# Kernel tuning notes

Measured on AMD Instinct MI355X. Metric: run time of the kernel, lower is better.

## Reference

```python
import jax, jax.numpy as jnp
import numpy as np

B, S, D, H = 2, 2048, 1024, 16
HD = D // H
WIN = 32
LN_EPS = 1e-5


def _ln(x, g, b):
    m = jnp.mean(x, axis=-1, keepdims=True)
    v = jnp.mean(jnp.square(x - m), axis=-1, keepdims=True)
    return (x - m) / jnp.sqrt(v + LN_EPS) * g + b


def setup_inputs() -> dict:
    key = jax.random.key(0)
    ks = jax.random.split(key, 12)
    def w(k, shape):
        return jax.random.normal(k, shape, dtype=jnp.float32) * 0.02
    inp = {
        'x': jax.random.normal(ks[0], (B, S, D), dtype=jnp.float32),
        'fq_w': w(ks[1], (D, D)), 'fq_b': jnp.zeros((D,), jnp.float32),
        'fk_w': w(ks[2], (D, D)), 'fk_b': jnp.zeros((D,), jnp.float32),
        'fv_w': w(ks[3], (D, D)), 'fv_b': jnp.zeros((D,), jnp.float32),
        'bq_w': w(ks[4], (D, D)), 'bq_b': jnp.zeros((D,), jnp.float32),
        'bk_w': w(ks[5], (D, D)), 'bk_b': jnp.zeros((D,), jnp.float32),
        'bv_w': w(ks[6], (D, D)), 'bv_b': jnp.zeros((D,), jnp.float32),
        'gate_w': w(ks[7], (2 * D, D)), 'gate_b': jnp.zeros((D,), jnp.float32),
        'gln_g': jnp.ones((D,), jnp.float32), 'gln_b': jnp.zeros((D,), jnp.float32),
        'bstr': jnp.asarray(0.1, jnp.float32),
        'out_w': w(ks[8], (D, D)), 'out_b': jnp.zeros((D,), jnp.float32),
        'ln_g': jnp.ones((D,), jnp.float32), 'ln_b': jnp.zeros((D,), jnp.float32),
    }
    return inp


def _heads(x, w, b):
    # [B,S,D] -> [B,H,S,HD]
    y = x @ w + b
    return y.reshape(B, S, H, HD).transpose(0, 2, 1, 3)


def _merge(x):
    return x.transpose(0, 2, 1, 3).reshape(B, S, D)


def _forward(x, fq_w, fq_b, fk_w, fk_b, fv_w, fv_b,
             bq_w, bq_b, bk_w, bk_b, bv_w, bv_b,
             gate_w, gate_b, gln_g, gln_b, bstr, out_w, out_b, ln_g, ln_b):
    scale = 1.0 / np.sqrt(HD)
    i = jnp.arange(S)
    # --- causal forward attention ---
    Q = _heads(x, fq_w, fq_b); K = _heads(x, fk_w, fk_b); V = _heads(x, fv_w, fv_b)
    scores = jnp.einsum('bhqd,bhkd->bhqk', Q, K) * scale
    causal = i[:, None] >= i[None, :]  # allowed positions
    scores = jnp.where(causal[None, None], scores, -jnp.inf)
    fwd = _merge(jnp.einsum('bhqk,bhkd->bhqd', jax.nn.softmax(scores, axis=-1), V))
    # --- limited-window backward attention (future_context = hidden_states) ---
    Qb = _heads(x, bq_w, bq_b); Kb = _heads(x, bk_w, bk_b); Vb = _heads(x, bv_w, bv_b)
    sb = jnp.einsum('bhqd,bhkd->bhqk', Qb, Kb) * scale
    valid = (i[None, :] > i[:, None]) & (i[None, :] <= i[:, None] + WIN)
    sb = jnp.where(valid[None, None], sb, -jnp.inf)
    # rows with no valid future (last row) get scores reset to 0 -> uniform softmax,
    # matching torch's all_masked handling
    row_valid = valid.any(axis=-1)  # [S]
    sb = jnp.where(row_valid[None, None, :, None], sb, 0.0)
    bwd = _merge(jnp.einsum('bhqk,bhkd->bhqd', jax.nn.softmax(sb, axis=-1), Vb))
    # --- weak gated fusion (eval mode: no dropout, backward detached) ---
    combined = jnp.concatenate([fwd, bwd], axis=-1)
    gate = jax.nn.sigmoid(_ln(combined @ gate_w + gate_b, gln_g, gln_b))
    strength = jax.nn.sigmoid(bstr) * 0.3
    fused = fwd + strength * gate * jax.lax.stop_gradient(bwd)
    out = fused @ out_w + out_b
    return _ln(x + out, ln_g, ln_b)


def reference(x, fq_w, fq_b, fk_w, fk_b, fv_w, fv_b,
              bq_w, bq_b, bk_w, bk_b, bv_w, bv_b,
              gate_w, gate_b, gln_g, gln_b, bstr, out_w, out_b, ln_g, ln_b):
    return _forward(x, fq_w, fq_b, fk_w, fk_b, fv_w, fv_b,
                    bq_w, bq_b, bk_w, bk_b, bv_w, bv_b,
                    gate_w, gate_b, gln_g, gln_b, bstr, out_w, out_b, ln_g, ln_b)
```

## Files before the change

kernel.cpp:

```cpp
#include <hip/hip_runtime.h>

#define S_LEN 2048
#define NH 16
#define HD 64
#define DMODEL 1024
#define NTOK 4096
#define ELTS_PER 4194304
#define QSCALE 0.18033688f

typedef __attribute__((ext_vector_type(8))) __bf16 bfrag;
typedef __attribute__((ext_vector_type(8))) short s8v;
typedef __attribute__((ext_vector_type(4))) float f32x4;

__device__ inline float bf2f(short s) {
  unsigned int u = ((unsigned int)(unsigned short)s) << 16;
  float f;
  __builtin_memcpy(&f, &u, 4);
  return f;
}
__device__ inline short f2bf(float f) {
  unsigned int u;
  __builtin_memcpy(&u, &f, 4);
  u = (u + 0x7fffu + ((u >> 16) & 1u)) >> 16;
  return (short)u;
}
__device__ inline short f2bf_n(float f) {
  __bf16 h = (__bf16)f;
  short s;
  __builtin_memcpy(&s, &h, 2);
  return s;
}
__device__ inline float bflo(unsigned int u) {
  unsigned int t = u << 16;
  float f; __builtin_memcpy(&f, &t, 4); return f;
}
__device__ inline float bfhi(unsigned int u) {
  unsigned int t = u & 0xffff0000u;
  float f; __builtin_memcpy(&f, &t, 4); return f;
}
__device__ __forceinline__ void gll16(const short* g, short* l) {
  __builtin_amdgcn_global_load_lds(
      (const __attribute__((address_space(1))) void*)g,
      (__attribute__((address_space(3))) void*)l, 16, 0, 0);
}

__global__ __launch_bounds__(256) void cvt_bf16_kernel(const float* __restrict__ in,
                                                       short* __restrict__ out, int n) {
  int i = (blockIdx.x * 256 + threadIdx.x) * 4;
  if (i + 3 < n) {
    float4 v = *reinterpret_cast<const float4*>(in + i);
    short4 o;
    o.x = f2bf(v.x); o.y = f2bf(v.y); o.z = f2bf(v.z); o.w = f2bf(v.w);
    *reinterpret_cast<short4*>(out + i) = o;
  }
}

__global__ void transpose_cvt_all(const float* __restrict__ s0, const float* __restrict__ s1,
                                  const float* __restrict__ s2, const float* __restrict__ s3,
                                  const float* __restrict__ s4, const float* __restrict__ s5,
                                  const float* __restrict__ s6, const float* __restrict__ s7,
                                  short* d0, short* d1, short* d2, short* d3,
                                  short* d4, short* d5, short* d6, short* d7) {
  const int z = blockIdx.z;
  const int K = (z == 7) ? 2048 : 1024;
  if (blockIdx.y * 32 >= K) return;
  const float* srcs[8] = {s0, s1, s2, s3, s4, s5, s6, s7};
  short* dsts[8] = {d0, d1, d2, d3, d4, d5, d6, d7};
  const float* in = srcs[z];
  short* out = dsts[z];
  __shared__ float tile[32][33];
  int nb = blockIdx.x * 32, kb = blockIdx.y * 32;
  int tx = threadIdx.x, ty = threadIdx.y;
  for (int j = 0; j < 32; j += 8)
    tile[ty + j][tx] = in[(size_t)(kb + ty + j) * 1024 + nb + tx];
  __syncthreads();
  for (int j = 0; j < 32; j += 8)
    out[(size_t)(nb + ty + j) * K + kb + tx] = f2bf(tile[tx][ty + j]);
}

__global__ __launch_bounds__(256) void gemm_qkv_kernel(
    const short* __restrict__ A, int lda, int K,
    const short* __restrict__ B0, const short* __restrict__ B1, const short* __restrict__ B2,
    const short* __restrict__ B3, const short* __restrict__ B4, const short* __restrict__ B5,
    const float* __restrict__ bias0, const float* __restrict__ bias1,
    const float* __restrict__ bias2, const float* __restrict__ bias3,
    const float* __restrict__ bias4, const float* __restrict__ bias5,
    short* __restrict__ outQ) {
  __shared__ short lds[128 * 136];
  short* As = lds;
  short* Bs = lds + 8192;
  const int tid = threadIdx.x;
  const int n0 = blockIdx.x * 128;
  const int m0 = blockIdx.y * 128;
  const short* Bp[6] = {B0, B1, B2, B3, B4, B5};
  const float* biasP[6] = {bias0, bias1, bias2, bias3, bias4, bias5};
  const int nsel = n0 >> 10;
  const int nc0 = n0 & 1023;
  const short* Bt = Bp[nsel] + (size_t)nc0 * K;
  const float* bsel = biasP[nsel];

  const int lane = tid & 63;
  const int w = tid >> 6;
  const int wm = (w >> 1) * 64;
  const int wn = (w & 1) * 64;
  const int lr = lane & 15;
  const int lg = lane >> 4;
  const int rl = lane >> 3;
  const int gch = (lane & 7) ^ (rl & 7);

  f32x4 acc[4][4];
  for (int a = 0; a < 4; ++a)
    for (int b = 0; b < 4; ++b) acc[a][b] = {0.f, 0.f, 0.f, 0.f};

  for (int k0 = 0; k0 < K; k0 += 64) {
    __syncthreads();
    for (int p = 0; p < 4; ++p) {
      int rb = (p * 4 + w) * 8;
      gll16(A + (size_t)(m0 + rb + rl) * lda + k0 + gch * 8, &As[rb * 64]);
      gll16(Bt + (size_t)(rb + rl) * K + k0 + gch * 8, &Bs[rb * 64]);
    }
    __syncthreads();
    for (int ks = 0; ks < 2; ++ks) {
      bfrag af[4], bf[4];
      for (int t = 0; t < 4; ++t) {
        af[t] = *reinterpret_cast<const bfrag*>(
            &As[(wm + t * 16 + lr) * 64 + (((lg + 4 * ks) ^ (lr & 7)) * 8)]);
        bf[t] = *reinterpret_cast<const bfrag*>(
            &Bs[(wn + t * 16 + lr) * 64 + (((lg + 4 * ks) ^ (lr & 7)) * 8)]);
      }
      for (int mt = 0; mt < 4; ++mt)
        for (int nt = 0; nt < 4; ++nt)
          acc[mt][nt] = __builtin_amdgcn_mfma_f32_16x16x32_bf16(af[mt], bf[nt], acc[mt][nt], 0, 0, 0);
    }
  }

  const float cmul = (nsel == 0 || nsel == 3) ? QSCALE : 1.0f;
  const bool tr = (nsel == 2 || nsel == 5);
  __syncthreads();
  for (int mt = 0; mt < 4; ++mt)
    for (int nt = 0; nt < 4; ++nt) {
      int c = wn + nt * 16 + lr;
      float bv = bsel[nc0 + c];
      for (int i = 0; i < 4; ++i) {
        int r = wm + mt * 16 + lg * 4 + i;
        short v16 = f2bf_n((acc[mt][nt][i] + bv) * cmul);
        if (tr) lds[c * 136 + r] = v16;
        else lds[r * 136 + c] = v16;
      }
    }
  __syncthreads();
  const int bb = m0 >> 11;
  const int sloc = m0 & 2047;
  const int hh0 = nc0 >> 6;
  short* basebuf = outQ + (size_t)nsel * ELTS_PER;
  for (int j = 0; j < 8; ++j) {
    int gid = j * 256 + tid;
    int rr = gid >> 4;
    int ch = gid & 15;
    s8v v = *reinterpret_cast<const s8v*>(&lds[rr * 136 + ch * 8]);
    if (tr) {
      int hh = hh0 + (rr >> 6), d = rr & 63;
      *reinterpret_cast<s8v*>(
          basebuf + ((size_t)(bb * NH + hh) * HD + d) * S_LEN + sloc + ch * 8) = v;
    } else {
      int hh = hh0 + (ch >> 3), d0 = (ch & 7) * 8;
      *reinterpret_cast<s8v*>(
          basebuf + ((size_t)(bb * NH + hh) * S_LEN + sloc + rr) * HD + d0) = v;
    }
  }
}

__global__ __launch_bounds__(256) void gemm_ksplit_kernel(
    const short* __restrict__ A0, const short* __restrict__ A1, int lda,
    const short* __restrict__ B, int ldb, int K,
    const float* __restrict__ bias, float* __restrict__ out0, float* __restrict__ out1) {
  __shared__ short lds[16384];
  short* As = lds;
  short* Bs = lds + 8192;
  const int tid = threadIdx.x;
  const int n0 = blockIdx.x * 128;
  const int m0 = blockIdx.y * 128;
  const int z = blockIdx.z;
  const short* A = z ? A1 : A0;
  const short* Bt = B + (size_t)n0 * ldb + z * K;
  float* outp = z ? out1 : out0;

  const int lane = tid & 63;
  const int w = tid >> 6;
  const int wm = (w >> 1) * 64;
  const int wn = (w & 1) * 64;
  const int lr = lane & 15;
  const int lg = lane >> 4;
  const int rl = lane >> 3;
  const int gch = (lane & 7) ^ (rl & 7);

  f32x4 acc[4][4];
  for (int a = 0; a < 4; ++a)
    for (int b = 0; b < 4; ++b) acc[a][b] = {0.f, 0.f, 0.f, 0.f};

  for (int k0 = 0; k0 < K; k0 += 64) {
    __syncthreads();
    for (int p = 0; p < 4; ++p) {
      int rb = (p * 4 + w) * 8;
      gll16(A + (size_t)(m0 + rb + rl) * lda + k0 + gch * 8, &As[rb * 64]);
      gll16(Bt + (size_t)(rb + rl) * ldb + k0 + gch * 8, &Bs[rb * 64]);
    }
    __syncthreads();
    for (int ks = 0; ks < 2; ++ks) {
      bfrag af[4], bf[4];
      for (int t = 0; t < 4; ++t) {
        af[t] = *reinterpret_cast<const bfrag*>(
            &As[(wm + t * 16 + lr) * 64 + (((lg + 4 * ks) ^ (lr & 7)) * 8)]);
        bf[t] = *reinterpret_cast<const bfrag*>(
            &Bs[(wn + t * 16 + lr) * 64 + (((lg + 4 * ks) ^ (lr & 7)) * 8)]);
      }
      for (int mt = 0; mt < 4; ++mt)
        for (int nt = 0; nt < 4; ++nt)
          acc[mt][nt] = __builtin_amdgcn_mfma_f32_16x16x32_bf16(af[mt], bf[nt], acc[mt][nt], 0, 0, 0);
    }
  }

  for (int mt = 0; mt < 4; ++mt)
    for (int nt = 0; nt < 4; ++nt)
      for (int i = 0; i < 4; ++i) {
        int row = m0 + wm + mt * 16 + lg * 4 + i;
        int col = n0 + wn + nt * 16 + lr;
        float v = acc[mt][nt][i] + (z == 0 ? bias[col] : 0.f);
        outp[(size_t)row * DMODEL + col] = v;
      }
}

__global__ __launch_bounds__(256) void attn_fwd_kernel(const short* __restrict__ Q,
                                                       const short* __restrict__ Kk,
                                                       const short* __restrict__ VT,
                                                       short* __restrict__ fwd) {
  __shared__ short Kls[64 * 64];
  __shared__ short Vls[64 * 64];
  __shared__ short Ps[4][32 * 72];
  const int tid = threadIdx.x;
  const int lane = tid & 63;
  const int w = tid >> 6;
  const int lr = lane & 15;
  const int lg = lane >> 4;
  const int f = blockIdx.x;
  const int xcd = f & 7;
  const int s = f >> 3;
  const int bhl = s & 3;
  const int t = s >> 2;
  const int j = (t < 8) ? t : (23 - t);
  const int bh = xcd * 4 + bhl;
  const int b = bh >> 4;
  const int h = bh & 15;
  const size_t hb = (size_t)bh * S_LEN * HD;
  short* Pw = Ps[w];

  s8v onesi = {0x3F80, 0x3F80, 0x3F80, 0x3F80, 0x3F80, 0x3F80, 0x3F80, 0x3F80};
  bfrag onesv;
  __builtin_memcpy(&onesv, &onesi, 16);

  const int q0 = j * 128 + w * 32;
  const int ktmax = 2 * j + 1;

  const int rl8 = lane >> 3;
  const int gch = (lane & 7) ^ rl8;

  bfrag qf[2][2];
  for (int mt = 0; mt < 2; ++mt)
    for (int kc = 0; kc < 2; ++kc)
      qf[mt][kc] = *reinterpret_cast<const bfrag*>(
          Q + hb + (size_t)(q0 + mt * 16 + lr) * HD + kc * 32 + lg * 8);

  f32x4 oacc[2][4];
  for (int mt = 0; mt < 2; ++mt)
    for (int nd = 0; nd < 4; ++nd) oacc[mt][nd] = {0.f, 0.f, 0.f, 0.f};
  f32x4 osum[2];
  osum[0] = {0.f, 0.f, 0.f, 0.f};
  osum[1] = {0.f, 0.f, 0.f, 0.f};

  for (int kt = 0; kt <= ktmax; ++kt) {
    __syncthreads();
    const short* Kg = Kk + hb + (size_t)(kt * 64 + w * 16 + rl8) * HD + gch * 8;
    gll16(Kg, &Kls[(w * 16) * 64]);
    gll16(Kg + (size_t)8 * HD, &Kls[(w * 16 + 8) * 64]);
    const short* Vg = VT + hb + (size_t)(w * 16 + rl8) * S_LEN + kt * 64 + gch * 8;
    gll16(Vg, &Vls[(w * 16) * 64]);
    gll16(Vg + (size_t)8 * S_LEN, &Vls[(w * 16 + 8) * 64]);
    __syncthreads();
    bfrag kf[4][2];
    for (int nb = 0; nb < 4; ++nb)
      for (int kc = 0; kc < 2; ++kc)
        kf[nb][kc] = *reinterpret_cast<const bfrag*>(
            &Kls[(nb * 16 + lr) * 64 + (((kc * 4 + lg) ^ (lr & 7)) * 8)]);
    f32x4 sv[2][4];
    for (int mt = 0; mt < 2; ++mt)
      for (int nb = 0; nb < 4; ++nb) {
        f32x4 z = {0.f, 0.f, 0.f, 0.f};
        z = __builtin_amdgcn_mfma_f32_16x16x32_bf16(qf[mt][0], kf[nb][0], z, 0, 0, 0);
        sv[mt][nb] = __builtin_amdgcn_mfma_f32_16x16x32_bf16(qf[mt][1], kf[nb][1], z, 0, 0, 0);
      }
    if (kt * 64 + 63 > q0) {
      for (int mt = 0; mt < 2; ++mt)
        for (int nb = 0; nb < 4; ++nb)
          for (int i = 0; i < 4; ++i) {
            int colg = kt * 64 + nb * 16 + lr;
            int rowg = q0 + mt * 16 + lg * 4 + i;
            if (colg > rowg) sv[mt][nb][i] = -1e30f;
          }
    }
    for (int mt = 0; mt < 2; ++mt)
      for (int nb = 0; nb < 4; ++nb)
        for (int i = 0; i < 4; ++i)
          Pw[(mt * 16 + lg * 4 + i) * 72 + nb * 16 + lr] = f2bf_n(exp2f(sv[mt][nb][i]));
    bfrag vf[4][2];
    for (int nd = 0; nd < 4; ++nd)
      for (int kc = 0; kc < 2; ++kc)
        vf[nd][kc] = *reinterpret_cast<const bfrag*>(
            &Vls[(nd * 16 + lr) * 64 + (((kc * 4 + lg) ^ (lr & 7)) * 8)]);
    for (int mt = 0; mt < 2; ++mt) {
      bfrag pa0 = *reinterpret_cast<const bfrag*>(&Pw[(mt * 16 + lr) * 72 + lg * 8]);
      bfrag pa1 = *reinterpret_cast<const bfrag*>(&Pw[(mt * 16 + lr) * 72 + 32 + lg * 8]);
      for (int nd = 0; nd < 4; ++nd) {
        oacc[mt][nd] = __builtin_amdgcn_mfma_f32_16x16x32_bf16(pa0, vf[nd][0], oacc[mt][nd], 0, 0, 0);
        oacc[mt][nd] = __builtin_amdgcn_mfma_f32_16x16x32_bf16(pa1, vf[nd][1], oacc[mt][nd], 0, 0, 0);
      }
      osum[mt] = __builtin_amdgcn_mfma_f32_16x16x32_bf16(pa0, onesv, osum[mt], 0, 0, 0);
      osum[mt] = __builtin_amdgcn_mfma_f32_16x16x32_bf16(pa1, onesv, osum[mt], 0, 0, 0);
    }
  }

  for (int mt = 0; mt < 2; ++mt)
    for (int i = 0; i < 4; ++i) {
      int rowg = q0 + mt * 16 + lg * 4 + i;
      float inv = 1.0f / osum[mt][i];
      for (int nd = 0; nd < 4; ++nd)
        fwd[(size_t)(b * S_LEN + rowg) * DMODEL + h * HD + nd * 16 + lr] =
            f2bf(oacc[mt][nd][i] * inv);
    }
}

__global__ __launch_bounds__(256) void attn_bwd_kernel(const short* __restrict__ Qb,
                                                       const short* __restrict__ Kb,
                                                       const short* __restrict__ VT,
                                                       short* __restrict__ bwd) {
  __shared__ short Ps[4][32 * 72];
  const int tid = threadIdx.x;
  const int lane = tid & 63;
  const int w = tid >> 6;
  const int lr = lane & 15;
  const int lg = lane >> 4;
  const int h = blockIdx.y;
  const int b = blockIdx.z;
  const size_t hb = (size_t)(b * NH + h) * S_LEN * HD;
  const int q0 = blockIdx.x * 128 + w * 32;
  short* Pw = Ps[w];

  bfrag qf[2][2];
  for (int mt = 0; mt < 2; ++mt)
    for (int kc = 0; kc < 2; ++kc)
      qf[mt][kc] = *reinterpret_cast<const bfrag*>(
          Qb + hb + (size_t)(q0 + mt * 16 + lr) * HD + kc * 32 + lg * 8);
  bfrag kf[4][2];
  for (int nb = 0; nb < 4; ++nb) {
    int kr = q0 + nb * 16 + lr;
    kr = min(kr, S_LEN - 1);
    for (int kc = 0; kc < 2; ++kc)
      kf[nb][kc] = *reinterpret_cast<const bfrag*>(
          Kb + hb + (size_t)kr * HD + kc * 32 + lg * 8);
  }
  f32x4 sv[2][4];
  for (int mt = 0; mt < 2; ++mt)
    for (int nb = 0; nb < 4; ++nb) {
      f32x4 z = {0.f, 0.f, 0.f, 0.f};
      z = __builtin_amdgcn_mfma_f32_16x16x32_bf16(qf[mt][0], kf[nb][0], z, 0, 0, 0);
      sv[mt][nb] = __builtin_amdgcn_mfma_f32_16x16x32_bf16(qf[mt][1], kf[nb][1], z, 0, 0, 0);
    }
  float mx[2][4];
  for (int mt = 0; mt < 2; ++mt)
    for (int i = 0; i < 4; ++i) {
      int rowg = q0 + mt * 16 + lg * 4 + i;
      float m = -1e30f;
      for (int nb = 0; nb < 4; ++nb) {
        int colg = q0 + nb * 16 + lr;
        float t = sv[mt][nb][i];
        bool valid = (colg > rowg) && (colg <= rowg + 32) && (colg < S_LEN);
        if (!valid) t = -1e30f;
        sv[mt][nb][i] = t;
        m = fmaxf(m, t);
      }
      mx[mt][i] = m;
    }
  for (int off = 1; off < 16; off <<= 1)
    for (int mt = 0; mt < 2; ++mt)
      for (int i = 0; i < 4; ++i) mx[mt][i] = fmaxf(mx[mt][i], __shfl_xor(mx[mt][i], off));
  float rs[2][4] = {{0.f, 0.f, 0.f, 0.f}, {0.f, 0.f, 0.f, 0.f}};
  for (int mt = 0; mt < 2; ++mt)
    for (int nb = 0; nb < 4; ++nb)
      for (int i = 0; i < 4; ++i) {
        float p = exp2f(sv[mt][nb][i] - mx[mt][i]);
        rs[mt][i] += p;
        Pw[(mt * 16 + lg * 4 + i) * 72 + nb * 16 + lr] = f2bf_n(p);
      }
  for (int off = 1; off < 16; off <<= 1)
    for (int mt = 0; mt < 2; ++mt)
      for (int i = 0; i < 4; ++i) rs[mt][i] += __shfl_xor(rs[mt][i], off);
  bfrag vf[4][2];
  for (int nd = 0; nd < 4; ++nd)
    for (int kc = 0; kc < 2; ++kc) {
      int sbase = q0 + kc * 32 + lg * 8;
      sbase = min(sbase, S_LEN - 8);
      vf[nd][kc] = *reinterpret_cast<const bfrag*>(
          VT + hb + (size_t)(nd * 16 + lr) * S_LEN + sbase);
    }
  f32x4 oacc[2][4];
  for (int mt = 0; mt < 2; ++mt)
    for (int nd = 0; nd < 4; ++nd) oacc[mt][nd] = {0.f, 0.f, 0.f, 0.f};
  for (int mt = 0; mt < 2; ++mt) {
    bfrag pa0 = *reinterpret_cast<const bfrag*>(&Pw[(mt * 16 + lr) * 72 + lg * 8]);
    bfrag pa1 = *reinterpret_cast<const bfrag*>(&Pw[(mt * 16 + lr) * 72 + 32 + lg * 8]);
    for (int nd = 0; nd < 4; ++nd) {
      oacc[mt][nd] = __builtin_amdgcn_mfma_f32_16x16x32_bf16(pa0, vf[nd][0], oacc[mt][nd], 0, 0, 0);
      oacc[mt][nd] = __builtin_amdgcn_mfma_f32_16x16x32_bf16(pa1, vf[nd][1], oacc[mt][nd], 0, 0, 0);
    }
  }
  for (int mt = 0; mt < 2; ++mt)
    for (int nd = 0; nd < 4; ++nd)
      for (int i = 0; i < 4; ++i) {
        int rowg = q0 + mt * 16 + lg * 4 + i;
        float ov = oacc[mt][nd][i] / rs[mt][i];
        bwd[(size_t)(b * S_LEN + rowg) * DMODEL + h * HD + nd * 16 + lr] = f2bf(ov);
      }
}

__global__ __launch_bounds__(256) void vmean_kernel(const short* __restrict__ VT,
                                                    short* __restrict__ bwd) {
  __shared__ float red[256];
  const int bh = blockIdx.x;
  const int d = threadIdx.x >> 2;
  const int seg = threadIdx.x & 3;
  const short* row = VT + (size_t)bh * S_LEN * HD + (size_t)d * S_LEN + seg * 512;
  float s = 0.f;
  for (int j = 0; j < 512; j += 8) {
    uint4 v = *reinterpret_cast<const uint4*>(row + j);
    s += bflo(v.x) + bfhi(v.x) + bflo(v.y) + bfhi(v.y) +
         bflo(v.z) + bfhi(v.z) + bflo(v.w) + bfhi(v.w);
  }
  red[threadIdx.x] = s;
  __syncthreads();
  if (seg == 0) {
    float t = red[d * 4] + red[d * 4 + 1] + red[d * 4 + 2] + red[d * 4 + 3];
    int b = bh >> 4, h = bh & 15;
    bwd[((size_t)(b * S_LEN + S_LEN - 1)) * DMODEL + h * HD + d] = f2bf(t * (1.f / S_LEN));
  }
}

__global__ __launch_bounds__(256) void ln_gate_fuse_kernel(
    const float* __restrict__ g0p, const float* __restrict__ g1p,
    const float* __restrict__ gln_g, const float* __restrict__ gln_b,
    const short* __restrict__ fwd, const short* __restrict__ bwd,
    const float* __restrict__ bstr, short* __restrict__ fused) {
  __shared__ float red[8];
  const int row = blockIdx.x;
  const int tid = threadIdx.x;
  const int lane = tid & 63;
  const int w = tid >> 6;
  float4 x0 = *reinterpret_cast<const float4*>(g0p + (size_t)row * DMODEL + tid * 4);
  float4 x1 = *reinterpret_cast<const float4*>(g1p + (size_t)row * DMODEL + tid * 4);
  float xa[4] = {x0.x + x1.x, x0.y + x1.y, x0.z + x1.z, x0.w + x1.w};
  float s = xa[0] + xa[1] + xa[2] + xa[3];
  float ss = xa[0] * xa[0] + xa[1] * xa[1] + xa[2] * xa[2] + xa[3] * xa[3];
  for (int off = 1; off < 64; off <<= 1) {
    s += __shfl_xor(s, off);
    ss += __shfl_xor(ss, off);
  }
  if (lane == 0) { red[w] = s; red[4 + w] = ss; }
  __syncthreads();
  s = red[0] + red[1] + red[2] + red[3];
  ss = red[4] + red[5] + red[6] + red[7];
  const float mean = s * (1.f / DMODEL);
  const float var = ss * (1.f / DMODEL) - mean * mean;
  const float rstd = rsqrtf(var + 1e-5f);
  const float strength = 0.3f / (1.f + __expf(-bstr[0]));
  for (int e = 0; e < 4; ++e) {
    int idx = tid * 4 + e;
    float g = (xa[e] - mean) * rstd * gln_g[idx] + gln_b[idx];
    float gate = 1.f / (1.f + __expf(-g));
    float f = bf2f(fwd[(size_t)row * DMODEL + idx]) +
              strength * gate * bf2f(bwd[(size_t)row * DMODEL + idx]);
    fused[(size_t)row * DMODEL + idx] = f2bf(f);
  }
}

__global__ __launch_bounds__(256) void final_ln_kernel(const float* __restrict__ x,
                                                       const float* __restrict__ o0p,
                                                       const float* __restrict__ o1p,
                                                       const float* __restrict__ ln_g,
                                                       const float* __restrict__ ln_b,
                                                       float* __restrict__ y) {
  __shared__ float red[8];
  const int row = blockIdx.x;
  const int tid = threadIdx.x;
  const int lane = tid & 63;
  const int w = tid >> 6;
  float4 xv = *reinterpret_cast<const float4*>(x + (size_t)row * DMODEL + tid * 4);
  float4 o0 = *reinterpret_cast<const float4*>(o0p + (size_t)row * DMODEL + tid * 4);
  float4 o1 = *reinterpret_cast<const float4*>(o1p + (size_t)row * DMODEL + tid * 4);
  float t[4] = {xv.x + o0.x + o1.x, xv.y + o0.y + o1.y,
                xv.z + o0.z + o1.z, xv.w + o0.w + o1.w};
  float s = t[0] + t[1] + t[2] + t[3];
  float ss = t[0] * t[0] + t[1] * t[1] + t[2] * t[2] + t[3] * t[3];
  for (int off = 1; off < 64; off <<= 1) {
    s += __shfl_xor(s, off);
    ss += __shfl_xor(ss, off);
  }
  if (lane == 0) { red[w] = s; red[4 + w] = ss; }
  __syncthreads();
  s = red[0] + red[1] + red[2] + red[3];
  ss = red[4] + red[5] + red[6] + red[7];
  const float mean = s * (1.f / DMODEL);
  const float var = ss * (1.f / DMODEL) - mean * mean;
  const float rstd = rsqrtf(var + 1e-5f);
  for (int e = 0; e < 4; ++e) {
    int idx = tid * 4 + e;
    y[(size_t)row * DMODEL + idx] = (t[e] - mean) * rstd * ln_g[idx] + ln_b[idx];
  }
}

extern "C" void kernel_launch(void* const* d_in, const int* in_sizes, int n_in,
                              void* d_out, int out_size, void* d_ws, size_t ws_size,
                              hipStream_t stream) {
  const float* x = (const float*)d_in[0];
  const float* fq_w = (const float*)d_in[1];
  const float* fq_b = (const float*)d_in[2];
  const float* fk_w = (const float*)d_in[3];
  const float* fk_b = (const float*)d_in[4];
  const float* fv_w = (const float*)d_in[5];
  const float* fv_b = (const float*)d_in[6];
  const float* bq_w = (const float*)d_in[7];
  const float* bq_b = (const float*)d_in[8];
  const float* bk_w = (const float*)d_in[9];
  const float* bk_b = (const float*)d_in[10];
  const float* bv_w = (const float*)d_in[11];
  const float* bv_b = (const float*)d_in[12];
  const float* gate_w = (const float*)d_in[13];
  const float* gate_b = (const float*)d_in[14];
  const float* gln_g = (const float*)d_in[15];
  const float* gln_b = (const float*)d_in[16];
  const float* bstr = (const float*)d_in[17];
  const float* out_w = (const float*)d_in[18];
  const float* out_b = (const float*)d_in[19];
  const float* ln_g = (const float*)d_in[20];
  const float* ln_b = (const float*)d_in[21];

  char* ws = (char*)d_ws;
  const size_t MB = 1u << 20;
  short* xb = (short*)(ws + 0);
  short* wT0 = (short*)(ws + 8 * MB);
  short* wT1 = (short*)(ws + 10 * MB);
  short* wT2 = (short*)(ws + 12 * MB);
  short* wT3 = (short*)(ws + 14 * MB);
  short* wT4 = (short*)(ws + 16 * MB);
  short* wT5 = (short*)(ws + 18 * MB);
  short* gwT = (short*)(ws + 20 * MB);
  short* owT = (short*)(ws + 24 * MB);
  short* qkv = (short*)(ws + 26 * MB);
  short* fwd = (short*)(ws + 0);
  short* bwdb = (short*)(ws + 8 * MB);
  float* G0 = (float*)(ws + 26 * MB);
  float* G1 = (float*)(ws + 42 * MB);
  short* fused = (short*)(ws + 58 * MB);
  float* O0 = (float*)(ws + 26 * MB);
  float* O1 = (float*)(ws + 42 * MB);

  cvt_bf16_kernel<<<4096, 256, 0, stream>>>(x, xb, ELTS_PER);
  transpose_cvt_all<<<dim3(32, 64, 8), dim3(32, 8), 0, stream>>>(
      fq_w, fk_w, fv_w, bq_w, bk_w, bv_w, out_w, gate_w,
      wT0, wT1, wT2, wT3, wT4, wT5, owT, gwT);

  gemm_qkv_kernel<<<dim3(48, 32), 256, 0, stream>>>(
      xb, 1024, 1024, wT0, wT1, wT2, wT3, wT4, wT5,
      fq_b, fk_b, fv_b, bq_b, bk_b, bv_b, qkv);

  attn_fwd_kernel<<<512, 256, 0, stream>>>(
      qkv, qkv + (size_t)ELTS_PER, qkv + 2 * (size_t)ELTS_PER, fwd);
  attn_bwd_kernel<<<dim3(16, 16, 2), 256, 0, stream>>>(
      qkv + 3 * (size_t)ELTS_PER, qkv + 4 * (size_t)ELTS_PER, qkv + 5 * (size_t)ELTS_PER, bwdb);
  vmean_kernel<<<32, 256, 0, stream>>>(qkv + 5 * (size_t)ELTS_PER, bwdb);

  gemm_ksplit_kernel<<<dim3(8, 32, 2), 256, 0, stream>>>(
      fwd, bwdb, 1024, gwT, 2048, 1024, gate_b, G0, G1);

  ln_gate_fuse_kernel<<<4096, 256, 0, stream>>>(G0, G1, gln_g, gln_b, fwd, bwdb, bstr, fused);

  gemm_ksplit_kernel<<<dim3(8, 32, 2), 256, 0, stream>>>(
      fused, fused + 512, 1024, owT, 1024, 512, out_b, O0, O1);

  final_ln_kernel<<<4096, 256, 0, stream>>>(x, O0, O1, ln_g, ln_b, (float*)d_out);
}
```

Baseline: 250.9 us.

## Double-buffer LDS tiles in GEMM and forward attention kernels

The QKV and k-split GEMMs move from a single 64-wide K tile to double-buffered 32-wide K tiles, with a new XOR swizzle. The next tile is prefetched with global-to-LDS loads while MFMAs run on the current one, leaving one barrier per iteration instead of two. The causal forward attention kernel likewise double-buffers its K/V tiles to overlap loads with compute. The cost is twice the LDS for attention K/V and twice as many loop iterations with less MFMA work each in the GEMMs, which could raise barrier overhead.

After: 261.6 us. 1.04x slower.

```diff
diff --git a/kernel.cpp b/kernel.cpp
--- a/kernel.cpp
+++ b/kernel.cpp
@@ -87,8 +87,6 @@
     const float* __restrict__ bias4, const float* __restrict__ bias5,
     short* __restrict__ outQ) {
   __shared__ short lds[128 * 136];
-  short* As = lds;
-  short* Bs = lds + 8192;
   const int tid = threadIdx.x;
   const int n0 = blockIdx.x * 128;
   const int m0 = blockIdx.y * 128;
@@ -105,38 +103,46 @@
   const int wn = (w & 1) * 64;
   const int lr = lane & 15;
   const int lg = lane >> 4;
-  const int rl = lane >> 3;
-  const int gch = (lane & 7) ^ (rl & 7);
+  const int gr = lane >> 2;
+  const int gs = (((lane & 3) ^ ((gr >> 1) & 3)) * 8);
+  const int rsw = (lr >> 1) & 3;
 
   f32x4 acc[4][4];
   for (int a = 0; a < 4; ++a)
     for (int b = 0; b < 4; ++b) acc[a][b] = {0.f, 0.f, 0.f, 0.f};
 
-  for (int k0 = 0; k0 < K; k0 += 64) {
+#define QKV_STAGE(K0, AD, BD)                                              \
+  do {                                                                     \
+    const short* Ag = A + (size_t)(m0 + w * 32 + gr) * lda + (K0) + gs;    \
+    gll16(Ag, (AD) + (w * 32) * 32);                                       \
+    gll16(Ag + (size_t)16 * lda, (AD) + (w * 32 + 16) * 32);               \
+    const short* Bg = Bt + (size_t)(w * 32 + gr) * K + (K0) + gs;          \
+    gll16(Bg, (BD) + (w * 32) * 32);                                       \
+    gll16(Bg + (size_t)16 * K, (BD) + (w * 32 + 16) * 32);                 \
+  } while (0)
+
+  QKV_STAGE(0, lds, lds + 8192);
+  __syncthreads();
+  for (int k0 = 0; k0 < K; k0 += 32) {
+    const int cur = (k0 >> 5) & 1;
+    if (k0 + 32 < K)
+      QKV_STAGE(k0 + 32, lds + (cur ^ 1) * 4096, lds + 8192 + (cur ^ 1) * 4096);
+    const short* As = lds + cur * 4096;
+    const short* Bs = lds + 8192 + cur * 4096;
+    bfrag af[4], bf[4];
+    for (int t = 0; t < 4; ++t) {
+      af[t] = *reinterpret_cast<const bfrag*>(&As[(wm + t * 16 + lr) * 32 + ((lg ^ rsw) * 8)]);
+      bf[t] = *reinterpret_cast<const bfrag*>(&Bs[(wn + t * 16 + lr) * 32 + ((lg ^ rsw) * 8)]);
+    }
+    for (int mt = 0; mt < 4; ++mt)
+      for (int nt = 0; nt < 4; ++nt)
+        acc[mt][nt] = __builtin_amdgcn_mfma_f32_16x16x32_bf16(af[mt], bf[nt], acc[mt][nt], 0, 0, 0);
     __syncthreads();
-    for (int p = 0; p < 4; ++p) {
-      int rb = (p * 4 + w) * 8;
-      gll16(A + (size_t)(m0 + rb + rl) * lda + k0 + gch * 8, &As[rb * 64]);
-      gll16(Bt + (size_t)(rb + rl) * K + k0 + gch * 8, &Bs[rb * 64]);
-    }
-    __syncthreads();
-    for (int ks = 0; ks < 2; ++ks) {
-      bfrag af[4], bf[4];
-      for (int t = 0; t < 4; ++t) {
-        af[t] = *reinterpret_cast<const bfrag*>(
-            &As[(wm + t * 16 + lr) * 64 + (((lg + 4 * ks) ^ (lr & 7)) * 8)]);
-        bf[t] = *reinterpret_cast<const bfrag*>(
-            &Bs[(wn + t * 16 + lr) * 64 + (((lg + 4 * ks) ^ (lr & 7)) * 8)]);
-      }
-      for (int mt = 0; mt < 4; ++mt)
-        for (int nt = 0; nt < 4; ++nt)
-          acc[mt][nt] = __builtin_amdgcn_mfma_f32_16x16x32_bf16(af[mt], bf[nt], acc[mt][nt], 0, 0, 0);
-    }
-  }
+  }
+#undef QKV_STAGE
 
   const float cmul = (nsel == 0 || nsel == 3) ? QSCALE : 1.0f;
   const bool tr = (nsel == 2 || nsel == 5);
-  __syncthreads();
   for (int mt = 0; mt < 4; ++mt)
     for (int nt = 0; nt < 4; ++nt) {
       int c = wn + nt * 16 + lr;
@@ -175,8 +181,6 @@
     const short* __restrict__ B, int ldb, int K,
     const float* __restrict__ bias, float* __restrict__ out0, float* __restrict__ out1) {
   __shared__ short lds[16384];
-  short* As = lds;
-  short* Bs = lds + 8192;
   const int tid = threadIdx.x;
   const int n0 = blockIdx.x * 128;
   const int m0 = blockIdx.y * 128;
@@ -191,34 +195,43 @@
   const int wn = (w & 1) * 64;
   const int lr = lane & 15;
   const int lg = lane >> 4;
-  const int rl = lane >> 3;
-  const int gch = (lane & 7) ^ (rl & 7);
+  const int gr = lane >> 2;
+  const int gs = (((lane & 3) ^ ((gr >> 1) & 3)) * 8);
+  const int rsw = (lr >> 1) & 3;
 
   f32x4 acc[4][4];
   for (int a = 0; a < 4; ++a)
     for (int b = 0; b < 4; ++b) acc[a][b] = {0.f, 0.f, 0.f, 0.f};
 
-  for (int k0 = 0; k0 < K; k0 += 64) {
+#define KS_STAGE(K0, AD, BD)                                               \
+  do {                                                                     \
+    const short* Ag = A + (size_t)(m0 + w * 32 + gr) * lda + (K0) + gs;    \
+    gll16(Ag, (AD) + (w * 32) * 32);                                       \
+    gll16(Ag + (size_t)16 * lda, (AD) + (w * 32 + 16) * 32);               \
+    const short* Bg = Bt + (size_t)(w * 32 + gr) * ldb + (K0) + gs;        \
+    gll16(Bg, (BD) + (w * 32) * 32);                                       \
+    gll16(Bg + (size_t)16 * ldb, (BD) + (w * 32 + 16) * 32);               \
+  } while (0)
+
+  KS_STAGE(0, lds, lds + 8192);
+  __syncthreads();
+  for (int k0 = 0; k0 < K; k0 += 32) {
+    const int cur = (k0 >> 5) & 1;
+    if (k0 + 32 < K)
+      KS_STAGE(k0 + 32, lds + (cur ^ 1) * 4096, lds + 8192 + (cur ^ 1) * 4096);
+    const short* As = lds + cur * 4096;
+    const short* Bs = lds + 8192 + cur * 4096;
+    bfrag af[4], bf[4];
+    for (int t = 0; t < 4; ++t) {
+      af[t] = *reinterpret_cast<const bfrag*>(&As[(wm + t * 16 + lr) * 32 + ((lg ^ rsw) * 8)]);
+      bf[t] = *reinterpret_cast<const bfrag*>(&Bs[(wn + t * 16 + lr) * 32 + ((lg ^ rsw) * 8)]);
+    }
+    for (int mt = 0; mt < 4; ++mt)
+      for (int nt = 0; nt < 4; ++nt)
+        acc[mt][nt] = __builtin_amdgcn_mfma_f32_16x16x32_bf16(af[mt], bf[nt], acc[mt][nt], 0, 0, 0);
     __syncthreads();
-    for (int p = 0; p < 4; ++p) {
-      int rb = (p * 4 + w) * 8;
-      gll16(A + (size_t)(m0 + rb + rl) * lda + k0 + gch * 8, &As[rb * 64]);
-      gll16(Bt + (size_t)(rb + rl) * ldb + k0 + gch * 8, &Bs[rb * 64]);
-    }
-    __syncthreads();
-    for (int ks = 0; ks < 2; ++ks) {
-      bfrag af[4], bf[4];
-      for (int t = 0; t < 4; ++t) {
-        af[t] = *reinterpret_cast<const bfrag*>(
-            &As[(wm + t * 16 + lr) * 64 + (((lg + 4 * ks) ^ (lr & 7)) * 8)]);
-        bf[t] = *reinterpret_cast<const bfrag*>(
-            &Bs[(wn + t * 16 + lr) * 64 + (((lg + 4 * ks) ^ (lr & 7)) * 8)]);
-      }
-      for (int mt = 0; mt < 4; ++mt)
-        for (int nt = 0; nt < 4; ++nt)
-          acc[mt][nt] = __builtin_amdgcn_mfma_f32_16x16x32_bf16(af[mt], bf[nt], acc[mt][nt], 0, 0, 0);
-    }
-  }
+  }
+#undef KS_STAGE
 
   for (int mt = 0; mt < 4; ++mt)
     for (int nt = 0; nt < 4; ++nt)
@@ -234,8 +247,8 @@
                                                        const short* __restrict__ Kk,
                                                        const short* __restrict__ VT,
                                                        short* __restrict__ fwd) {
-  __shared__ short Kls[64 * 64];
-  __shared__ short Vls[64 * 64];
+  __shared__ short Kls[2][64 * 64];
+  __shared__ short Vls[2][64 * 64];
   __shared__ short Ps[4][32 * 72];
   const int tid = threadIdx.x;
   const int lane = tid & 63;
@@ -277,20 +290,29 @@
   osum[0] = {0.f, 0.f, 0.f, 0.f};
   osum[1] = {0.f, 0.f, 0.f, 0.f};
 
+#define AF_STAGE(KT, BUF)                                                            \
+  do {                                                                               \
+    const short* Kg = Kk + hb + (size_t)((KT) * 64 + w * 16 + rl8) * HD + gch * 8;   \
+    gll16(Kg, &Kls[BUF][(w * 16) * 64]);                                             \
+    gll16(Kg + (size_t)8 * HD, &Kls[BUF][(w * 16 + 8) * 64]);                        \
+    const short* Vg = VT + hb + (size_t)(w * 16 + rl8) * S_LEN + (KT) * 64 + gch * 8;\
+    gll16(Vg, &Vls[BUF][(w * 16) * 64]);                                             \
+    gll16(Vg + (size_t)8 * S_LEN, &Vls[BUF][(w * 16 + 8) * 64]);                     \
+  } while (0)
+
+  AF_STAGE(0, 0);
+  __syncthreads();
   for (int kt = 0; kt <= ktmax; ++kt) {
-    __syncthreads();
-    const short* Kg = Kk + hb + (size_t)(kt * 64 + w * 16 + rl8) * HD + gch * 8;
-    gll16(Kg, &Kls[(w * 16) * 64]);
-    gll16(Kg + (size_t)8 * HD, &Kls[(w * 16 + 8) * 64]);
-    const short* Vg = VT + hb + (size_t)(w * 16 + rl8) * S_LEN + kt * 64 + gch * 8;
-    gll16(Vg, &Vls[(w * 16) * 64]);
-    gll16(Vg + (size_t)8 * S_LEN, &Vls[(w * 16 + 8) * 64]);
-    __syncthreads();
+    const int cur = kt & 1;
+    if (kt < ktmax) {
+      if (cur == 0) AF_STAGE(kt + 1, 1);
+      else AF_STAGE(kt + 1, 0);
+    }
     bfrag kf[4][2];
     for (int nb = 0; nb < 4; ++nb)
       for (int kc = 0; kc < 2; ++kc)
         kf[nb][kc] = *reinterpret_cast<const bfrag*>(
-            &Kls[(nb * 16 + lr) * 64 + (((kc * 4 + lg) ^ (lr & 7)) * 8)]);
+            &Kls[cur][(nb * 16 + lr) * 64 + (((kc * 4 + lg) ^ (lr & 7)) * 8)]);
     f32x4 sv[2][4];
     for (int mt = 0; mt < 2; ++mt)
       for (int nb = 0; nb < 4; ++nb) {
@@ -315,7 +337,7 @@
     for (int nd = 0; nd < 4; ++nd)
       for (int kc = 0; kc < 2; ++kc)
         vf[nd][kc] = *reinterpret_cast<const bfrag*>(
-            &Vls[(nd * 16 + lr) * 64 + (((kc * 4 + lg) ^ (lr & 7)) * 8)]);
+            &Vls[cur][(nd * 16 + lr) * 64 + (((kc * 4 + lg) ^ (lr & 7)) * 8)]);
     for (int mt = 0; mt < 2; ++mt) {
       bfrag pa0 = *reinterpret_cast<const bfrag*>(&Pw[(mt * 16 + lr) * 72 + lg * 8]);
       bfrag pa1 = *reinterpret_cast<const bfrag*>(&Pw[(mt * 16 + lr) * 72 + 32 + lg * 8]);
@@ -326,7 +348,9 @@
       osum[mt] = __builtin_amdgcn_mfma_f32_16x16x32_bf16(pa0, onesv, osum[mt], 0, 0, 0);
       osum[mt] = __builtin_amdgcn_mfma_f32_16x16x32_bf16(pa1, onesv, osum[mt], 0, 0, 0);
     }
-  }
+    __syncthreads();
+  }
+#undef AF_STAGE
 
   for (int mt = 0; mt < 2; ++mt)
     for (int i = 0; i < 4; ++i) {
```
